# Optimization experiments

Measured on AMD Instinct MI355X. Metric: run time of the kernel, lower is better.

Reference implementation:

```python
import jax, jax.numpy as jnp
import numpy as np

EMBED_DIM = 1024
NUM_HEADS = 16
HEAD_DIM = EMBED_DIM // NUM_HEADS
# Source divides by scale = head_dim**-0.5, i.e. multiplies logits by sqrt(head_dim).
INV_SCALE = float(HEAD_DIM) ** 0.5


def setup_inputs() -> dict:
    key = jax.random.key(0)
    ks = jax.random.split(key, 9)
    E = EMBED_DIM
    s = 1.0 / np.sqrt(E)
    x = jax.random.normal(ks[0], (2, 2048, E), dtype=jnp.float32)
    Wq = jax.random.uniform(ks[1], (E, E), jnp.float32, -s, s)
    bq = jax.random.uniform(ks[2], (E,), jnp.float32, -s, s)
    Wk = jax.random.uniform(ks[3], (E, E), jnp.float32, -s, s)
    bk = jax.random.uniform(ks[4], (E,), jnp.float32, -s, s)
    Wv = jax.random.uniform(ks[5], (E, E), jnp.float32, -s, s)
    bv = jax.random.uniform(ks[6], (E,), jnp.float32, -s, s)
    Wo = jax.random.uniform(ks[7], (E, E), jnp.float32, -s, s)
    bo = jax.random.uniform(ks[8], (E,), jnp.float32, -s, s)
    return {"x": x, "Wq": Wq, "bq": bq, "Wk": Wk, "bk": bk,
            "Wv": Wv, "bv": bv, "Wo": Wo, "bo": bo}


def reference(x, Wq, bq, Wk, bk, Wv, bv, Wo, bo):
    B, N, C = x.shape
    H, D = NUM_HEADS, HEAD_DIM
    # nn.Linear: y = x @ W.T + b
    q = (x @ Wq.T + bq).reshape(B, N, H, D).transpose(0, 2, 1, 3)  # [B,H,N,D]
    k = (x @ Wk.T + bk).reshape(B, N, H, D).transpose(0, 2, 1, 3)
    v = (x @ Wv.T + bv).reshape(B, N, H, D).transpose(0, 2, 1, 3)
    # Faithful to source: logits = QK^T / (head_dim**-0.5) = QK^T * sqrt(head_dim)
    logits = jnp.einsum('bhnd,bhmd->bhnm', q, k) * INV_SCALE  # [B,H,N,N]
    attn = jax.nn.softmax(logits, axis=-1)
    h = jnp.einsum('bhnm,bhmd->bhnd', attn, v)  # [B,H,N,D]
    concat_h = h.transpose(0, 2, 1, 3).reshape(B, N, C)
    return concat_h @ Wo.T + bo
```

## Files before the change

kernel.cpp:

```cpp
#include <hip/hip_runtime.h>
#include <math.h>

#define B_ 2
#define N_ 2048
#define E_ 1024
#define H_ 16
#define D_ 64

typedef unsigned short US;
typedef _Float16 h16x8 __attribute__((ext_vector_type(8)));
typedef __fp16 fp16x2 __attribute__((ext_vector_type(2)));
typedef float f32x4 __attribute__((ext_vector_type(4)));
#define MFMA16F(a,b,c) __builtin_amdgcn_mfma_f32_16x16x32_f16(a,b,c,0,0,0)
#define SCL  11.5415603828f

union HU { _Float16 h; US u; };
__device__ __forceinline__ US f2h(float f){ HU x; x.h = (_Float16)f; return x.u; }
__device__ __forceinline__ unsigned pkrtz(float a, float b){
  union { fp16x2 h; unsigned u; } x;
  x.h = __builtin_amdgcn_cvt_pkrtz(a, b);
  return x.u;
}

union U8 { US u[8]; uint4 v; };
union U4 { US u[4]; uint2 v; };

__device__ __forceinline__ void glds16(const US* g, US* l){
  __builtin_amdgcn_global_load_lds(
    (const __attribute__((address_space(1))) unsigned int*)(const void*)g,
    (__attribute__((address_space(3))) unsigned int*)(void*)l, 16, 0, 0);
}

__global__ __launch_bounds__(256) void conv_all(
    const float* __restrict__ x,
    const float* __restrict__ w0, const float* __restrict__ w1,
    const float* __restrict__ w2, const float* __restrict__ w3,
    US* __restrict__ xh, US* __restrict__ Wall)
{
  const int id = blockIdx.x;
  const float* s; US* d; size_t off;
  if (id < 2048) { s = x; d = xh; off = (size_t)id*2048; }
  else {
    int j = id - 2048, wsel = j>>9;
    off = (size_t)(j&511)*2048;
    s = (wsel==0)?w0:(wsel==1)?w1:(wsel==2)?w2:w3;
    d = Wall + (size_t)wsel*1048576;
  }
  size_t i = off + (size_t)threadIdx.x*8;
  float f[8];
  *(float4*)&f[0] = *(const float4*)&s[i];
  *(float4*)&f[4] = *(const float4*)&s[i+4];
  U8 h;
  #pragma unroll
  for (int j=0;j<8;++j) h.u[j] = f2h(f[j]);
  *(uint4*)&d[i] = h.v;
}

__global__ __launch_bounds__(256,3) void qkv_gemm(
    const US* __restrict__ A, const US* __restrict__ Wall,
    const float* __restrict__ bq, const float* __restrict__ bk, const float* __restrict__ bv,
    US* __restrict__ Qf, US* __restrict__ Kf, US* __restrict__ Vtb)
{
  __shared__ __align__(16) US sA[128*32];
  __shared__ __align__(16) US sW[128*32];
  const int z = blockIdx.z;
  const US* W = Wall + (size_t)z*1048576;
  const float* bias = (z==0)?bq:(z==1)?bk:bv;

  const int t = threadIdx.x;
  const int w = t>>6, lane = t&63;
  const int q = lane>>4, c = lane&15;
  const int mq = (w>>1)*64, nq = (w&1)*64;
  const int gm0 = blockIdx.y*128, gn0 = blockIdx.x*128;
  const int r16 = lane>>2, seg = lane&3;

  f32x4 acc[4][4] = {};
  for (int kb = 0; kb < 1024; kb += 32) {
    #pragma unroll
    for (int p=0;p<2;++p){
      int rb = (w*2+p)*16;
      glds16(&A[(size_t)(gm0 + rb + r16)*1024 + kb + seg*8], &sA[rb*32]);
      glds16(&W[(size_t)(gn0 + rb + r16)*1024 + kb + seg*8], &sW[rb*32]);
    }
    __syncthreads();
    h16x8 af[4], wf[4];
    #pragma unroll
    for (int rt=0;rt<4;++rt) af[rt] = *(const h16x8*)&sA[(mq+rt*16+c)*32 + q*8];
    #pragma unroll
    for (int ct=0;ct<4;++ct) wf[ct] = *(const h16x8*)&sW[(nq+ct*16+c)*32 + q*8];
    #pragma unroll
    for (int rt=0;rt<4;++rt)
      #pragma unroll
      for (int ct=0;ct<4;++ct)
        acc[rt][ct] = MFMA16F(af[rt], wf[ct], acc[rt][ct]);
    __syncthreads();
  }
  #pragma unroll
  for (int rt=0;rt<4;++rt)
  #pragma unroll
  for (int ct=0;ct<4;++ct) {
    int col = gn0 + nq + ct*16 + c;
    float bv_ = bias[col];
    int rowb = gm0 + mq + rt*16 + q*4;
    int hh = col>>6, d = col & 63;
    if (z==2) {
      int b = rowb>>11, n = rowb & (N_-1);
      U4 pk;
      #pragma unroll
      for (int r=0;r<4;++r) pk.u[r] = f2h(acc[rt][ct][r] + bv_);
      *(uint2*)&Vtb[((size_t)(b*H_+hh)*D_ + d)*N_ + n] = pk.v;
    } else {
      US* dst = (z==0) ? Qf : Kf;
      #pragma unroll
      for (int r=0;r<4;++r) {
        int row = rowb + r;
        float v = acc[rt][ct][r] + bv_;
        if (z==0) v *= SCL;
        int b = row>>11, n = row & (N_-1);
        dst[((size_t)(b*H_+hh)*N_+n)*D_ + d] = f2h(v);
      }
    }
  }
}

__global__ __launch_bounds__(256,4) void o_gemm(
    const US* __restrict__ A, const US* __restrict__ W,
    const float* __restrict__ bias, float* __restrict__ out)
{
  __shared__ __align__(16) US sA[128*32];
  __shared__ __align__(16) US sW[64*32];
  const int t = threadIdx.x;
  const int w = t>>6, lane = t&63;
  const int q = lane>>4, c = lane&15;
  const int gm0 = blockIdx.y*128, gn0 = blockIdx.x*64;
  const int r16 = lane>>2, seg = lane&3;

  f32x4 acc[2][4] = {};
  for (int kb = 0; kb < 1024; kb += 32) {
    glds16(&A[(size_t)(gm0 + w*32      + r16)*1024 + kb + seg*8], &sA[(w*32)*32]);
    glds16(&A[(size_t)(gm0 + w*32 + 16 + r16)*1024 + kb + seg*8], &sA[(w*32+16)*32]);
    glds16(&W[(size_t)(gn0 + w*16      + r16)*1024 + kb + seg*8], &sW[(w*16)*32]);
    __syncthreads();
    h16x8 af0 = *(const h16x8*)&sA[(w*32+c)*32 + q*8];
    h16x8 af1 = *(const h16x8*)&sA[(w*32+16+c)*32 + q*8];
    #pragma unroll
    for (int ct=0; ct<4; ++ct){
      h16x8 wf = *(const h16x8*)&sW[(ct*16+c)*32 + q*8];
      acc[0][ct] = MFMA16F(af0, wf, acc[0][ct]);
      acc[1][ct] = MFMA16F(af1, wf, acc[1][ct]);
    }
    __syncthreads();
  }
  #pragma unroll
  for (int rt=0; rt<2; ++rt)
  #pragma unroll
  for (int ct=0; ct<4; ++ct) {
    int col = gn0 + ct*16 + c;
    float bv_ = bias[col];
    int rowb = gm0 + w*32 + rt*16 + q*4;
    #pragma unroll
    for (int r=0;r<4;++r)
      out[(size_t)(rowb+r)*1024 + col] = acc[rt][ct][r] + bv_;
  }
}

#define KSTR2 72
#define VSTR  136
__global__ __launch_bounds__(512,4) void attn(
    const US* __restrict__ Qf, const US* __restrict__ Kf, const US* __restrict__ Vt,
    US* __restrict__ Hout)
{
  __shared__ __align__(16) US sK [128*KSTR2];
  __shared__ __align__(16) US sVt[64*VSTR];
  __shared__ __align__(16) US sP [8][16*VSTR];
  const int t = threadIdx.x;
  const int w = t>>6, lane = t&63, q = lane>>4, c = lane&15;
  const int id = blockIdx.x;
  const int bh = ((id & 7) << 2) | ((id >> 3) & 3);
  const int n0 = (id >> 5) * 128;
  const US* Kp = Kf + (size_t)bh * (N_*D_);
  const US* Vp = Vt + (size_t)bh * (D_*N_);

  const size_t qoff = (size_t)bh*(N_*D_) + (size_t)(n0 + w*16 + c)*D_;
  h16x8 qb0 = *(const h16x8*)&Qf[qoff + q*8];
  h16x8 qb1 = *(const h16x8*)&Qf[qoff + 32 + q*8];
  h16x8 vones;
  #pragma unroll
  for (int j=0;j<8;++j) vones[j] = (_Float16)1.0f;

  float mi = -INFINITY;
  f32x4 o[5] = {};

  const int kr = t>>3, kc8 = (t&7)*8;
  const int vr = t>>4, vc8 = (t&15)*8;

  for (int mt=0; mt<16; ++mt) {
    const int m0 = mt*128;
    #pragma unroll
    for (int p=0;p<2;++p){
      int r = p*64 + kr;
      *(uint4*)&sK[r*KSTR2 + kc8] = *(const uint4*)&Kp[(size_t)(m0 + r)*D_ + kc8];
    }
    #pragma unroll
    for (int p=0;p<2;++p){
      int r = p*32 + vr;
      *(uint4*)&sVt[r*VSTR + vc8] = *(const uint4*)&Vp[(size_t)r*N_ + m0 + vc8];
    }
    __syncthreads();

    f32x4 s[8];
    #pragma unroll
    for (int f=0; f<8; ++f){
      h16x8 k0 = *(const h16x8*)&sK[(f*16+c)*KSTR2 + q*8];
      h16x8 k1 = *(const h16x8*)&sK[(f*16+c)*KSTR2 + 32 + q*8];
      f32x4 sv = {};
      sv = MFMA16F(k0, qb0, sv);
      sv = MFMA16F(k1, qb1, sv);
      s[f] = sv;
    }

    f32x4 vm = s[0];
    #pragma unroll
    for (int f=1; f<8; ++f){
      vm[0]=fmaxf(vm[0],s[f][0]); vm[1]=fmaxf(vm[1],s[f][1]);
      vm[2]=fmaxf(vm[2],s[f][2]); vm[3]=fmaxf(vm[3],s[f][3]);
    }
    float v = fmaxf(fmaxf(vm[0],vm[1]), fmaxf(vm[2],vm[3]));
    v = fmaxf(v, __shfl_xor(v, 16));
    v = fmaxf(v, __shfl_xor(v, 32));
    float mnew = fmaxf(mi, v);
    if (!__all(v <= mi)) {
      float alpha = exp2f(mi-mnew);
      float ar[4];
      #pragma unroll
      for (int r=0; r<4; ++r) ar[r] = __shfl(alpha, q*4+r);
      #pragma unroll
      for (int dt=0; dt<5; ++dt){
        o[dt][0]*=ar[0]; o[dt][1]*=ar[1]; o[dt][2]*=ar[2]; o[dt][3]*=ar[3];
      }
    }
    mi = mnew;
    #pragma unroll
    for (int f=0; f<8; ++f){
      float p0 = exp2f(s[f][0]-mnew);
      float p1 = exp2f(s[f][1]-mnew);
      float p2 = exp2f(s[f][2]-mnew);
      float p3 = exp2f(s[f][3]-mnew);
      uint2 pk;
      pk.x = pkrtz(p0, p1);
      pk.y = pkrtz(p2, p3);
      *(uint2*)&sP[w][c*VSTR + f*16 + q*4] = pk;
    }
    h16x8 pa[4];
    #pragma unroll
    for (int kc=0; kc<4; ++kc)
      pa[kc] = *(const h16x8*)&sP[w][c*VSTR + kc*32 + q*8];

    #pragma unroll
    for (int dt=0; dt<4; ++dt){
      #pragma unroll
      for (int kc=0; kc<4; ++kc){
        h16x8 vf = *(const h16x8*)&sVt[(dt*16+c)*VSTR + kc*32 + q*8];
        o[dt] = MFMA16F(pa[kc], vf, o[dt]);
      }
    }
    #pragma unroll
    for (int kc=0; kc<4; ++kc)
      o[4] = MFMA16F(pa[kc], vones, o[4]);
    __syncthreads();
  }

  const int b = bh>>4, hh = bh&15;
  float ir[4];
  #pragma unroll
  for (int r=0; r<4; ++r) ir[r] = 1.0f / o[4][r];
  #pragma unroll
  for (int dt=0; dt<4; ++dt){
    #pragma unroll
    for (int r=0; r<4; ++r){
      int n = n0 + w*16 + q*4 + r;
      int d = dt*16 + c;
      Hout[((size_t)(b*N_+n)*H_+hh)*D_ + d] = f2h(o[dt][r] * ir[r]);
    }
  }
}

extern "C" void kernel_launch(void* const* d_in, const int* in_sizes, int n_in,
                              void* d_out, int out_size, void* d_ws, size_t ws_size,
                              hipStream_t stream)
{
  const float* x  = (const float*)d_in[0];
  const float* Wq = (const float*)d_in[1];
  const float* bq = (const float*)d_in[2];
  const float* Wk = (const float*)d_in[3];
  const float* bk = (const float*)d_in[4];
  const float* Wv = (const float*)d_in[5];
  const float* bv = (const float*)d_in[6];
  const float* Wo = (const float*)d_in[7];
  const float* bo = (const float*)d_in[8];
  US* ws  = (US*)d_ws;
  const size_t M1 = 1048576;
  US* xh   = ws;
  US* Wall = ws + 4*M1;
  US* Qf   = ws + 8*M1;
  US* Kf   = ws + 12*M1;
  US* Vtb  = ws + 16*M1;
  US* Hf   = ws + 20*M1;

  conv_all<<<4096, 256, 0, stream>>>(x, Wq, Wk, Wv, Wo, xh, Wall);
  qkv_gemm<<<dim3(8,32,3), 256, 0, stream>>>(xh, Wall, bq, bk, bv, Qf, Kf, Vtb);
  attn<<<512, 512, 0, stream>>>(Qf, Kf, Vtb, Hf);
  o_gemm<<<dim3(16,32), 256, 0, stream>>>(Hf, Wall + 3*M1, bo, (float*)d_out);
}
```

Before: 209.0 us.

## Feed softmax probabilities to PV MFMA directly from registers, dropping LDS staging

Removes the per-wave shared-memory buffer for P by using the 16x16x16 MFMA, whose A-operand layout matches the S accumulator layout, so exponentiated probabilities go straight from registers into the PV product. This drops an LDS write/read round trip per tile and frees shared memory, allowing launch bounds to ask for more resident blocks per CU. It also adds s_setprio around MFMA sections to favour matrix issue across waves. The trade-off is twice as many smaller MFMA instructions and narrower 8-byte V fragment loads.

After: 223.5 us. 1.07x slower.

```diff
diff --git a/kernel.cpp b/kernel.cpp
--- a/kernel.cpp
+++ b/kernel.cpp
@@ -9,9 +9,11 @@
 
 typedef unsigned short US;
 typedef _Float16 h16x8 __attribute__((ext_vector_type(8)));
+typedef _Float16 h16x4 __attribute__((ext_vector_type(4)));
 typedef __fp16 fp16x2 __attribute__((ext_vector_type(2)));
 typedef float f32x4 __attribute__((ext_vector_type(4)));
-#define MFMA16F(a,b,c) __builtin_amdgcn_mfma_f32_16x16x32_f16(a,b,c,0,0,0)
+#define MFMA16F(a,b,c)  __builtin_amdgcn_mfma_f32_16x16x32_f16(a,b,c,0,0,0)
+#define MFMA161(a,b,c)  __builtin_amdgcn_mfma_f32_16x16x16f16(a,b,c,0,0,0)
 #define SCL  11.5415603828f
 
 union HU { _Float16 h; US u; };
@@ -24,6 +26,7 @@
 
 union U8 { US u[8]; uint4 v; };
 union U4 { US u[4]; uint2 v; };
+union UPA { unsigned u[2]; h16x4 h; };
 
 __device__ __forceinline__ void glds16(const US* g, US* l){
   __builtin_amdgcn_global_load_lds(
@@ -166,13 +169,12 @@
 
 #define KSTR2 72
 #define VSTR  136
-__global__ __launch_bounds__(512,4) void attn(
+__global__ __launch_bounds__(512,6) void attn(
     const US* __restrict__ Qf, const US* __restrict__ Kf, const US* __restrict__ Vt,
     US* __restrict__ Hout)
 {
   __shared__ __align__(16) US sK [128*KSTR2];
   __shared__ __align__(16) US sVt[64*VSTR];
-  __shared__ __align__(16) US sP [8][16*VSTR];
   const int t = threadIdx.x;
   const int w = t>>6, lane = t&63, q = lane>>4, c = lane&15;
   const int id = blockIdx.x;
@@ -184,9 +186,9 @@
   const size_t qoff = (size_t)bh*(N_*D_) + (size_t)(n0 + w*16 + c)*D_;
   h16x8 qb0 = *(const h16x8*)&Qf[qoff + q*8];
   h16x8 qb1 = *(const h16x8*)&Qf[qoff + 32 + q*8];
-  h16x8 vones;
-  #pragma unroll
-  for (int j=0;j<8;++j) vones[j] = (_Float16)1.0f;
+  h16x4 vones;
+  #pragma unroll
+  for (int j=0;j<4;++j) vones[j] = (_Float16)1.0f;
 
   float mi = -INFINITY;
   f32x4 o[5] = {};
@@ -209,6 +211,7 @@
     __syncthreads();
 
     f32x4 s[8];
+    __builtin_amdgcn_s_setprio(1);
     #pragma unroll
     for (int f=0; f<8; ++f){
       h16x8 k0 = *(const h16x8*)&sK[(f*16+c)*KSTR2 + q*8];
@@ -218,6 +221,7 @@
       sv = MFMA16F(k1, qb1, sv);
       s[f] = sv;
     }
+    __builtin_amdgcn_s_setprio(0);
 
     f32x4 vm = s[0];
     #pragma unroll
@@ -246,27 +250,19 @@
       float p1 = exp2f(s[f][1]-mnew);
       float p2 = exp2f(s[f][2]-mnew);
       float p3 = exp2f(s[f][3]-mnew);
-      uint2 pk;
-      pk.x = pkrtz(p0, p1);
-      pk.y = pkrtz(p2, p3);
-      *(uint2*)&sP[w][c*VSTR + f*16 + q*4] = pk;
-    }
-    h16x8 pa[4];
-    #pragma unroll
-    for (int kc=0; kc<4; ++kc)
-      pa[kc] = *(const h16x8*)&sP[w][c*VSTR + kc*32 + q*8];
-
-    #pragma unroll
-    for (int dt=0; dt<4; ++dt){
-      #pragma unroll
-      for (int kc=0; kc<4; ++kc){
-        h16x8 vf = *(const h16x8*)&sVt[(dt*16+c)*VSTR + kc*32 + q*8];
-        o[dt] = MFMA16F(pa[kc], vf, o[dt]);
+      UPA pa;
+      pa.u[0] = pkrtz(p0, p1);
+      pa.u[1] = pkrtz(p2, p3);
+      h16x4 pah = pa.h;
+      __builtin_amdgcn_s_setprio(1);
+      #pragma unroll
+      for (int dt=0; dt<4; ++dt){
+        h16x4 vf = *(const h16x4*)&sVt[(dt*16+c)*VSTR + f*16 + q*4];
+        o[dt] = MFMA161(pah, vf, o[dt]);
       }
-    }
-    #pragma unroll
-    for (int kc=0; kc<4; ++kc)
-      o[4] = MFMA16F(pa[kc], vones, o[4]);
+      o[4] = MFMA161(pah, vones, o[4]);
+      __builtin_amdgcn_s_setprio(0);
+    }
     __syncthreads();
   }
 
```
